# Kernel tuning notes

Hardware: AMD Instinct MI355X
Metric: run time of the kernel (lower is better)

Reference implementation:

```python
import jax, jax.numpy as jnp
import numpy as np

B, S, HID, NH, CACHE = 2, 1024, 1024, 16, 4096
HD = HID // NH
HOT = max(4, CACHE // 4)
COLD = CACHE - HOT
COMP = HID // 2
EPS = 1e-5


def setup_inputs() -> dict:
    key = jax.random.key(0)
    ks = jax.random.split(key, 16)
    std = 0.02
    inp = {
        'inputs': jax.random.normal(ks[0], (B, S, HID), jnp.float32),
        'hot_keys': std * jax.random.normal(ks[1], (HOT, HID), jnp.float32),
        'hot_values': std * jax.random.normal(ks[2], (HOT, HID), jnp.float32),
        'hot_age': jnp.zeros((HOT,), jnp.float32),
        'hot_access': jnp.zeros((HOT,), jnp.float32),
        'cold_keys': std * jax.random.normal(ks[3], (COLD, HID), jnp.float32),
        'cold_values': std * jax.random.normal(ks[4], (COLD, HID), jnp.float32),
        'cold_age': jnp.zeros((COLD,), jnp.float32),
        'cold_access': jnp.zeros((COLD,), jnp.float32),
        # linear weights stored [in, out] (y = x @ W + b)
        'Wq': std * jax.random.normal(ks[5], (HID, HID), jnp.float32),
        'bq': jnp.zeros((HID,), jnp.float32),
        'Wk': std * jax.random.normal(ks[6], (HID, HID), jnp.float32),
        'bk': jnp.zeros((HID,), jnp.float32),
        'Wv': std * jax.random.normal(ks[7], (HID, HID), jnp.float32),
        'bv': jnp.zeros((HID,), jnp.float32),
        'Wo': std * jax.random.normal(ks[8], (HID, HID), jnp.float32),
        'bo': jnp.zeros((HID,), jnp.float32),
        'Wc': (1.0 / np.sqrt(HID)) * jax.random.normal(ks[9], (HID, COMP), jnp.float32),
        'bc': jnp.zeros((COMP,), jnp.float32),
        'Wd': (1.0 / np.sqrt(COMP)) * jax.random.normal(ks[10], (COMP, HID), jnp.float32),
        'bd': jnp.zeros((HID,), jnp.float32),
        'gamma': jnp.ones((HID,), jnp.float32),
        'beta': jnp.zeros((HID,), jnp.float32),
    }
    return inp


def _cache_level(q, cache_k, v_flat, age, access, Wk, bk, Wo, bo):
    # q: [B, NH, S, HD]; cache_k/v_flat: [C, HID]
    C = cache_k.shape[0]
    k = (cache_k @ Wk + bk).reshape(C, NH, HD)
    v = v_flat.reshape(C, NH, HD)
    scores = jnp.einsum('bhsd,chd->bhsc', q, k) / np.sqrt(HD)
    scores = scores + (-0.1 * age + 0.05 * access)  # broadcast over [B,H,S,C]
    attn = jax.nn.softmax(scores, axis=-1)
    out = jnp.einsum('bhsc,chd->bhsd', attn, v)
    out = out.transpose(0, 2, 1, 3).reshape(q.shape[0], q.shape[2], HID)
    return out @ Wo + bo


def reference(inputs, hot_keys, hot_values, hot_age, hot_access,
              cold_keys, cold_values, cold_age, cold_access,
              Wq, bq, Wk, bk, Wv, bv, Wo, bo, Wc, bc, Wd, bd, gamma, beta):
    q = (inputs @ Wq + bq).reshape(B, S, NH, HD).transpose(0, 2, 1, 3)
    # hot tier: values through value_net
    hot_v = hot_values @ Wv + bv
    hot_out = _cache_level(q, hot_keys, hot_v, hot_age, hot_access, Wk, bk, Wo, bo)
    # cold tier: values through compressor -> decompressor
    cold_v = (cold_values @ Wc + bc) @ Wd + bd
    cold_out = _cache_level(q, cold_keys, cold_v, cold_age, cold_access, Wk, bk, Wo, bo)
    x = hot_out + cold_out
    mu = jnp.mean(x, axis=-1, keepdims=True)
    var = jnp.mean(jnp.square(x - mu), axis=-1, keepdims=True)
    return (x - mu) / jnp.sqrt(var + EPS) * gamma + beta
```

## Files before the change

### kernel.cpp

```cpp
#include <hip/hip_runtime.h>

#define BBATCH 2
#define SS   1024
#define HID  1024
#define NH   16
#define HD   64
#define HOT  1024
#define COLD 3072
#define COMP 512

typedef __attribute__((ext_vector_type(8))) short s8v;
typedef __attribute__((ext_vector_type(4))) float f4v;
typedef unsigned short u16;
typedef unsigned int   u32;

__device__ __forceinline__ float b2f(u16 u){ return __uint_as_float(((u32)u)<<16); }
__device__ __forceinline__ u16 f2b(float f){
  u32 u = __float_as_uint(f);
  u += 0x7FFF + ((u>>16)&1);
  return (u16)(u>>16);
}
__device__ __forceinline__ u32 pk2r(u32 a, u32 b){
  return __builtin_amdgcn_perm(b + 0x8000u, a + 0x8000u, 0x07060302u);
}
__device__ __forceinline__ float ldsc(const void* p, int i, int isf32){
  return isf32 ? ((const float*)p)[i] : b2f(((const u16*)p)[i]);
}

__global__ void detect_kernel(const u32* __restrict__ gamma_raw, u32* __restrict__ flag){
  if (threadIdx.x == 0) flag[0] = (gamma_raw[0] == 0x3F800000u) ? 1u : 0u;
}

__global__ __launch_bounds__(256) void bias_kernel(
    const void* __restrict__ h_age, const void* __restrict__ h_acc,
    const void* __restrict__ c_age, const void* __restrict__ c_acc,
    float* __restrict__ BiasH, float* __restrict__ BiasC, const u32* __restrict__ flag)
{
  const int f = (int)flag[0];
  const int i = blockIdx.x * 256 + threadIdx.x;
  if (i < HOT) BiasH[i] = -0.1f * ldsc(h_age, i, f) + 0.05f * ldsc(h_acc, i, f);
  const int j = i - HOT;
  if (j >= 0 && j < COLD) BiasC[j] = -0.1f * ldsc(c_age, j, f) + 0.05f * ldsc(c_acc, j, f);
}

struct CDesc { const void* S; u16* D; int tile0, pad; };
struct CBatch { CDesc d[5]; int nd; };

__global__ __launch_bounds__(256) void convert_multi(CBatch cb, const u32* __restrict__ flag)
{
  int di = 0;
  for (int i = 1; i < cb.nd; i++) if ((int)blockIdx.x >= cb.d[i].tile0) di = i;
  const CDesc g = cb.d[di];
  const int f = (int)flag[0];
  const size_t e0 = (size_t)(blockIdx.x - g.tile0) * 2048 + (size_t)threadIdx.x * 8;
  if (f) {
    const float* s = (const float*)g.S + e0;
    const uint4 x = *(const uint4*)s, y = *(const uint4*)(s + 4);
    *(uint4*)(g.D + e0) =
      (uint4){ pk2r(x.x,x.y), pk2r(x.z,x.w), pk2r(y.x,y.y), pk2r(y.z,y.w) };
  } else {
    *(uint4*)(g.D + e0) = *(const uint4*)((const u16*)g.S + e0);
  }
}

struct TDesc { const void* S; u16* D; int R, C, cshift, tile0; };
struct TBatch { TDesc d[6]; int nd; };

__global__ __launch_bounds__(256) void transpose_kernel(TBatch tb, const u32* __restrict__ flag)
{
  __shared__ __align__(16) u16 Tt[64][72];
  int di = 0;
  for (int i = 1; i < tb.nd; i++) if ((int)blockIdx.x >= tb.d[i].tile0) di = i;
  const TDesc g = tb.d[di];
  const int local = blockIdx.x - g.tile0;
  const int ty = local >> g.cshift;
  const int tx = local & ((1 << g.cshift) - 1);
  const int r0 = ty * 64, c0 = tx * 64;
  const int f = (int)flag[0];
  const int t = threadIdx.x;
  const int sr = t >> 2, sc = (t & 3) * 16;

  union { uint4 q[2]; u16 h[16]; } u;
  if (f) {
    const float* s = (const float*)g.S + (size_t)(r0 + sr) * g.C + c0 + sc;
    const uint4 a = *(const uint4*)s,     b = *(const uint4*)(s + 4);
    const uint4 c = *(const uint4*)(s + 8), d2 = *(const uint4*)(s + 12);
    u.q[0] = (uint4){ pk2r(a.x,a.y), pk2r(a.z,a.w), pk2r(b.x,b.y), pk2r(b.z,b.w) };
    u.q[1] = (uint4){ pk2r(c.x,c.y), pk2r(c.z,c.w), pk2r(d2.x,d2.y), pk2r(d2.z,d2.w) };
  } else {
    const u16* s = (const u16*)g.S + (size_t)(r0 + sr) * g.C + c0 + sc;
    u.q[0] = *(const uint4*)s;  u.q[1] = *(const uint4*)(s + 8);
  }
  #pragma unroll
  for (int i = 0; i < 16; i++) Tt[sc + i][sr] = u.h[i];
  __syncthreads();

  const int dc = t >> 2, dr = (t & 3) * 16;
  const uint4 o0 = *(const uint4*)&Tt[dc][dr];
  const uint4 o1 = *(const uint4*)&Tt[dc][dr + 8];
  u16* dp = g.D + (size_t)(c0 + dc) * g.R + r0 + dr;
  *(uint4*)dp = o0;  *(uint4*)(dp + 8) = o1;
}

#define BM 128
#define BN 64
#define BK 32
struct GemmDesc {
  const void* A; const u16* BT; const void* bias; u16* C;
  int aflag, bcol0, M, N, K, nxlog, tile0, ctrans;
  float bias_scale;
};
struct GemmBatch { GemmDesc d[6]; int nd; };

__global__ __launch_bounds__(256) void gemm_multi(GemmBatch bat, const u32* __restrict__ flag)
{
  __shared__ __align__(16) u16 As[BM][BK + 8];
  __shared__ __align__(16) u16 Bs[BN][BK + 8];

  int di = 0;
  for (int i = 1; i < bat.nd; i++) if ((int)blockIdx.x >= bat.d[i].tile0) di = i;
  const GemmDesc g = bat.d[di];
  const int local = blockIdx.x - g.tile0;
  const int ty = local >> g.nxlog;
  const int tx = local - (ty << g.nxlog);
  const int m0 = ty * BM, n0 = tx * BN;

  const int f  = (int)flag[0];
  const int af = g.aflag ? f : 0;

  const int tid  = threadIdx.x;
  const int lane = tid & 63, wave = tid >> 6;
  const int quad = lane >> 4, l15 = lane & 15;
  const int wy = wave >> 1, wx = wave & 1;

  f4v acc[4][2];
  #pragma unroll
  for (int i = 0; i < 4; i++)
    #pragma unroll
    for (int j = 0; j < 2; j++) acc[i][j] = (f4v){0.f,0.f,0.f,0.f};

  const int ar = tid >> 1, ac = (tid & 1) * 16;
  const int br = tid >> 2, bc = (tid & 3) * 8;

  uint4 a0, a1, a2, a3;
  uint4 b0;

  auto load_tile = [&](int kk) {
    if (af) {
      const float* s = (const float*)g.A + (size_t)(m0 + ar) * g.K + kk + ac;
      a0 = *(const uint4*)s;       a1 = *(const uint4*)(s + 4);
      a2 = *(const uint4*)(s + 8); a3 = *(const uint4*)(s + 12);
    } else {
      const u16* s = (const u16*)g.A + (size_t)(m0 + ar) * g.K + kk + ac;
      a0 = *(const uint4*)s;  a1 = *(const uint4*)(s + 8);
    }
    const u16* bs = g.BT + (size_t)(g.bcol0 + n0 + br) * g.K + kk + bc;
    b0 = *(const uint4*)bs;
  };

  load_tile(0);

  for (int k0 = 0; k0 < g.K; k0 += BK) {
    __syncthreads();
    if (af) {
      *(uint4*)&As[ar][ac] =
        (uint4){ pk2r(a0.x,a0.y), pk2r(a0.z,a0.w), pk2r(a1.x,a1.y), pk2r(a1.z,a1.w) };
      *(uint4*)&As[ar][ac + 8] =
        (uint4){ pk2r(a2.x,a2.y), pk2r(a2.z,a2.w), pk2r(a3.x,a3.y), pk2r(a3.z,a3.w) };
    } else {
      *(uint4*)&As[ar][ac] = a0;  *(uint4*)&As[ar][ac + 8] = a1;
    }
    *(uint4*)&Bs[br][bc] = b0;
    __syncthreads();

    if (k0 + BK < g.K) load_tile(k0 + BK);

    s8v afr[4], bfr[2];
    #pragma unroll
    for (int i = 0; i < 4; i++)
      afr[i] = *(const s8v*)&As[wy * 64 + i * 16 + l15][quad * 8];
    #pragma unroll
    for (int j = 0; j < 2; j++)
      bfr[j] = *(const s8v*)&Bs[wx * 32 + j * 16 + l15][quad * 8];

    #pragma unroll
    for (int j = 0; j < 2; j++)
      #pragma unroll
      for (int i = 0; i < 4; i++)
        acc[i][j] = __builtin_amdgcn_mfma_f32_16x16x32_bf16(afr[i], bfr[j], acc[i][j], 0, 0, 0);
  }

  if (g.ctrans) {
    #pragma unroll
    for (int j = 0; j < 2; j++) {
      const int col = n0 + wx * 32 + j * 16 + l15;
      const float bv = ldsc(g.bias, g.bcol0 + col, f) * g.bias_scale;
      #pragma unroll
      for (int i = 0; i < 4; i++) {
        const int row = m0 + wy * 64 + i * 16 + quad * 4;
        u16 t4[4];
        #pragma unroll
        for (int r = 0; r < 4; r++) t4[r] = f2b(acc[i][j][r] + bv);
        *(uint2*)&g.C[(size_t)col * g.M + row] = *(uint2*)t4;
      }
    }
  } else {
    #pragma unroll
    for (int j = 0; j < 2; j++) {
      const int col = n0 + wx * 32 + j * 16 + l15;
      const float bv = ldsc(g.bias, g.bcol0 + col, f) * g.bias_scale;
      #pragma unroll
      for (int i = 0; i < 4; i++) {
        const int row = m0 + wy * 64 + i * 16 + quad * 4;
        #pragma unroll
        for (int r = 0; r < 4; r++)
          g.C[(size_t)(row + r) * g.N + col] = f2b(acc[i][j][r] + bv);
      }
    }
  }
}

#define KV(row, blk) (((row) << 6) + ((((blk) ^ ((row) & 7))) << 3))

__global__ __launch_bounds__(256) void attn_kernel(
    const u16* __restrict__ Q,
    const u16* __restrict__ KHg, const u16* __restrict__ VHT,
    const u16* __restrict__ KCg, const u16* __restrict__ VCT,
    const float* __restrict__ BiasH, const float* __restrict__ BiasC,
    float* __restrict__ HotOut, float* __restrict__ ColdNum3, float* __restrict__ ColdZ3,
    int NG, int glog)
{
  __shared__ __align__(16) u16 Ks[64 * 64];
  __shared__ __align__(16) u16 Vs[64 * 64];

  const int tid  = threadIdx.x;
  const int lane = tid & 63, wave = tid >> 6;
  const int quad = lane >> 4, l15 = lane & 15;

  const int bx    = blockIdx.x;
  const int slice = bx & 3;
  const int sblk  = (bx >> 2) & 7;
  const int h     = (bx >> 5) & ((1 << glog) - 1);
  const int b     = bx >> (5 + glog);

  const int rowbase = b * SS + sblk * 128;
  const int hoff  = h * HD;
  const int myrow = wave * 32;

  const bool hot = (slice == 0);
  const u16*  Kt   = hot ? KHg : KCg;
  const u16*  Vt   = hot ? VHT : VCT;
  const float* Bias = hot ? BiasH : BiasC;
  const int   e0  = hot ? 0 : (slice - 1) * 1024;
  const int   ldv = hot ? HOT : COLD;

  const u16* qp = Q + (size_t)(rowbase + myrow + l15) * NG + hoff + quad * 8;
  const s8v aq0 = *(const s8v*)qp;
  const s8v aq1 = *(const s8v*)(qp + 32);
  const u16* qp1 = qp + (size_t)16 * NG;
  const s8v aq2 = *(const s8v*)qp1;
  const s8v aq3 = *(const s8v*)(qp1 + 32);

  const int rk = tid >> 2, cb2 = (tid & 3) * 2, sk = (tid & 3) * 16;
  const u16* kbase = Kt + (size_t)(e0 + rk) * NG + hoff + sk;
  const u16* vbase = Vt + (size_t)(hoff + rk) * ldv + e0 + sk;
  uint4 kr0 = *(const uint4*)kbase, kr1 = *(const uint4*)(kbase + 8);
  uint4 vr0 = *(const uint4*)vbase, vr1 = *(const uint4*)(vbase + 8);

  u16* kw0 = &Ks[KV(rk, cb2)];     u16* kw1 = &Ks[KV(rk, cb2 + 1)];
  u16* vw0 = &Vs[KV(rk, cb2)];     u16* vw1 = &Vs[KV(rk, cb2 + 1)];

  f4v o0[4], o1[4];
  #pragma unroll
  for (int j = 0; j < 4; j++) { o0[j] = (f4v){0.f,0.f,0.f,0.f}; o1[j] = (f4v){0.f,0.f,0.f,0.f}; }
  float zs0 = 0.f, zs1 = 0.f;

  for (int c0 = 0; c0 < 1024; c0 += 64) {
    __syncthreads();
    *(uint4*)kw0 = kr0;  *(uint4*)kw1 = kr1;
    *(uint4*)vw0 = vr0;  *(uint4*)vw1 = vr1;
    __syncthreads();
    if (c0 + 64 < 1024) {
      const u16* kn = kbase + (size_t)(c0 + 64) * NG;
      const u16* vn = vbase + (c0 + 64);
      kr0 = *(const uint4*)kn;  kr1 = *(const uint4*)(kn + 8);
      vr0 = *(const uint4*)vn;  vr1 = *(const uint4*)(vn + 8);
    }

    #pragma unroll
    for (int h2 = 0; h2 < 2; h2++) {
      const s8v ka0 = *(const s8v*)&Ks[KV(h2 * 32 + l15, quad)];
      const s8v ka1 = *(const s8v*)&Ks[KV(h2 * 32 + l15, 4 + quad)];
      const s8v kb0 = *(const s8v*)&Ks[KV(h2 * 32 + 16 + l15, quad)];
      const s8v kb1 = *(const s8v*)&Ks[KV(h2 * 32 + 16 + l15, 4 + quad)];

      const int cg0 = e0 + c0 + h2 * 32 + quad * 4;
      const float4 bi0 = *(const float4*)&Bias[cg0];
      const float4 bi1 = *(const float4*)&Bias[cg0 + 16];

      union { u32 w[4]; s8v v; } ap0, ap1;
      {
        f4v s0 = (f4v){0.f,0.f,0.f,0.f}, s1 = (f4v){0.f,0.f,0.f,0.f};
        s0 = __builtin_amdgcn_mfma_f32_16x16x32_bf16(ka0, aq0, s0, 0, 0, 0);
        s0 = __builtin_amdgcn_mfma_f32_16x16x32_bf16(ka1, aq1, s0, 0, 0, 0);
        s1 = __builtin_amdgcn_mfma_f32_16x16x32_bf16(kb0, aq0, s1, 0, 0, 0);
        s1 = __builtin_amdgcn_mfma_f32_16x16x32_bf16(kb1, aq1, s1, 0, 0, 0);
        float p0[4], p1[4];
        p0[0] = __expf(fminf(s0[0] * 0.125f + bi0.x, 30.f));
        p0[1] = __expf(fminf(s0[1] * 0.125f + bi0.y, 30.f));
        p0[2] = __expf(fminf(s0[2] * 0.125f + bi0.z, 30.f));
        p0[3] = __expf(fminf(s0[3] * 0.125f + bi0.w, 30.f));
        p1[0] = __expf(fminf(s1[0] * 0.125f + bi1.x, 30.f));
        p1[1] = __expf(fminf(s1[1] * 0.125f + bi1.y, 30.f));
        p1[2] = __expf(fminf(s1[2] * 0.125f + bi1.z, 30.f));
        p1[3] = __expf(fminf(s1[3] * 0.125f + bi1.w, 30.f));
        zs0 += p0[0] + p0[1] + p0[2] + p0[3] + p1[0] + p1[1] + p1[2] + p1[3];
        const u32 W0 = pk2r(__float_as_uint(p0[0]), __float_as_uint(p0[1]));
        const u32 W1 = pk2r(__float_as_uint(p0[2]), __float_as_uint(p0[3]));
        const u32 W2 = pk2r(__float_as_uint(p1[0]), __float_as_uint(p1[1]));
        const u32 W3 = pk2r(__float_as_uint(p1[2]), __float_as_uint(p1[3]));
        #pragma unroll
        for (int t = 0; t < 4; t++) {
          const int srcl = (((quad << 1) + (t >> 1)) & 3) * 16 + l15;
          const u32 lo = __shfl((t & 1) ? W1 : W0, srcl, 64);
          const u32 hi = __shfl((t & 1) ? W3 : W2, srcl, 64);
          ap0.w[t] = (quad >= 2) ? hi : lo;
        }
      }
      {
        f4v s0 = (f4v){0.f,0.f,0.f,0.f}, s1 = (f4v){0.f,0.f,0.f,0.f};
        s0 = __builtin_amdgcn_mfma_f32_16x16x32_bf16(ka0, aq2, s0, 0, 0, 0);
        s0 = __builtin_amdgcn_mfma_f32_16x16x32_bf16(ka1, aq3, s0, 0, 0, 0);
        s1 = __builtin_amdgcn_mfma_f32_16x16x32_bf16(kb0, aq2, s1, 0, 0, 0);
        s1 = __builtin_amdgcn_mfma_f32_16x16x32_bf16(kb1, aq3, s1, 0, 0, 0);
        float p0[4], p1[4];
        p0[0] = __expf(fminf(s0[0] * 0.125f + bi0.x, 30.f));
        p0[1] = __expf(fminf(s0[1] * 0.125f + bi0.y, 30.f));
        p0[2] = __expf(fminf(s0[2] * 0.125f + bi0.z, 30.f));
        p0[3] = __expf(fminf(s0[3] * 0.125f + bi0.w, 30.f));
        p1[0] = __expf(fminf(s1[0] * 0.125f + bi1.x, 30.f));
        p1[1] = __expf(fminf(s1[1] * 0.125f + bi1.y, 30.f));
        p1[2] = __expf(fminf(s1[2] * 0.125f + bi1.z, 30.f));
        p1[3] = __expf(fminf(s1[3] * 0.125f + bi1.w, 30.f));
        zs1 += p0[0] + p0[1] + p0[2] + p0[3] + p1[0] + p1[1] + p1[2] + p1[3];
        const u32 W0 = pk2r(__float_as_uint(p0[0]), __float_as_uint(p0[1]));
        const u32 W1 = pk2r(__float_as_uint(p0[2]), __float_as_uint(p0[3]));
        const u32 W2 = pk2r(__float_as_uint(p1[0]), __float_as_uint(p1[1]));
        const u32 W3 = pk2r(__float_as_uint(p1[2]), __float_as_uint(p1[3]));
        #pragma unroll
        for (int t = 0; t < 4; t++) {
          const int srcl = (((quad << 1) + (t >> 1)) & 3) * 16 + l15;
          const u32 lo = __shfl((t & 1) ? W1 : W0, srcl, 64);
          const u32 hi = __shfl((t & 1) ? W3 : W2, srcl, 64);
          ap1.w[t] = (quad >= 2) ? hi : lo;
        }
      }
      #pragma unroll
      for (int j2 = 0; j2 < 4; j2++) {
        const s8v bv = *(const s8v*)&Vs[KV(j2 * 16 + l15, h2 * 4 + quad)];
        o0[j2] = __builtin_amdgcn_mfma_f32_16x16x32_bf16(ap0.v, bv, o0[j2], 0, 0, 0);
        o1[j2] = __builtin_amdgcn_mfma_f32_16x16x32_bf16(ap1.v, bv, o1[j2], 0, 0, 0);
      }
    }
  }

  zs0 += __shfl_xor(zs0, 16, 64);  zs0 += __shfl_xor(zs0, 32, 64);
  zs1 += __shfl_xor(zs1, 16, 64);  zs1 += __shfl_xor(zs1, 32, 64);

  if (hot) {
    float rz0[4], rz1[4];
    #pragma unroll
    for (int r = 0; r < 4; r++) {
      rz0[r] = 1.0f / __shfl(zs0, quad * 4 + r, 64);
      rz1[r] = 1.0f / __shfl(zs1, quad * 4 + r, 64);
    }
    #pragma unroll
    for (int j = 0; j < 4; j++) {
      const int col = hoff + j * 16 + l15;
      #pragma unroll
      for (int r = 0; r < 4; r++) {
        const int row = rowbase + myrow + quad * 4 + r;
        HotOut[(size_t)row * NG + col]        = o0[j][r] * rz0[r];
        HotOut[(size_t)(row + 16) * NG + col] = o1[j][r] * rz1[r];
      }
    }
  } else {
    float* CN = ColdNum3 + (size_t)(slice - 1) * 2048 * NG;
    #pragma unroll
    for (int j = 0; j < 4; j++) {
      const int col = hoff + j * 16 + l15;
      #pragma unroll
      for (int r = 0; r < 4; r++) {
        const int row = rowbase + myrow + quad * 4 + r;
        CN[(size_t)row * NG + col]        = o0[j][r];
        CN[(size_t)(row + 16) * NG + col] = o1[j][r];
      }
    }
    if (lane < 16) {
      const size_t zb = (size_t)(slice - 1) * 2048 + rowbase + myrow;
      ColdZ3[(zb + lane) * (1 << glog) + h]      = zs0;
      ColdZ3[(zb + 16 + lane) * (1 << glog) + h] = zs1;
    }
  }
}

__global__ __launch_bounds__(256) void combine_kernel(
    const float* __restrict__ HotOut, const float* __restrict__ ColdNum3,
    const float* __restrict__ ColdZ3, u16* __restrict__ ATT,
    int att_ld, int att_c0, int NG, int glog)
{
  const int gid   = blockIdx.x * 256 + threadIdx.x;
  const int shift = 4 + glog;
  const int row   = gid >> shift;
  const int c4    = (gid & ((1 << shift) - 1)) << 2;
  const int h     = c4 >> 6;
  const int G     = 1 << glog;
  const size_t ps = (size_t)2048 * NG;
  const size_t zs = (size_t)2048 * G;

  const float4 hv = *(const float4*)&HotOut[(size_t)row * NG + c4];
  const float4 c1 = *(const float4*)&ColdNum3[(size_t)row * NG + c4];
  const float4 c2 = *(const float4*)&ColdNum3[ps + (size_t)row * NG + c4];
  const float4 c3 = *(const float4*)&ColdNum3[2 * ps + (size_t)row * NG + c4];
  const float z = ColdZ3[(size_t)row * G + h] + ColdZ3[zs + (size_t)row * G + h]
                + ColdZ3[2 * zs + (size_t)row * G + h];
  const float zi = 1.0f / z;

  u16 ov[4];
  ov[0] = f2b(hv.x + (c1.x + c2.x + c3.x) * zi);
  ov[1] = f2b(hv.y + (c1.y + c2.y + c3.y) * zi);
  ov[2] = f2b(hv.z + (c1.z + c2.z + c3.z) * zi);
  ov[3] = f2b(hv.w + (c1.w + c2.w + c3.w) * zi);
  *(uint2*)&ATT[(size_t)row * att_ld + att_c0 + c4] = *(uint2*)ov;
}

__global__ __launch_bounds__(256) void ln_kernel(
    const u16* __restrict__ X, const void* __restrict__ gamma,
    const void* __restrict__ beta, void* __restrict__ outp,
    const u32* __restrict__ flag)
{
  __shared__ float red[4];
  const int f = (int)flag[0];
  const int row = blockIdx.x, tid = threadIdx.x;
  const u16* xr = X + (size_t)row * HID;

  float x[4];
  { union { uint2 q; u16 hx[4]; } bx2;
    bx2.q = *(const uint2*)(xr + tid * 4);
    #pragma unroll
    for (int i = 0; i < 4; i++) x[i] = b2f(bx2.hx[i]); }

  float s = x[0] + x[1] + x[2] + x[3];
  #pragma unroll
  for (int m = 1; m < 64; m <<= 1) s += __shfl_xor(s, m, 64);
  if ((tid & 63) == 0) red[tid >> 6] = s;
  __syncthreads();
  const float mu = (red[0] + red[1] + red[2] + red[3]) * (1.0f / HID);
  __syncthreads();

  float v = 0.f;
  #pragma unroll
  for (int i = 0; i < 4; i++) { const float d = x[i] - mu; v += d * d; }
  #pragma unroll
  for (int m = 1; m < 64; m <<= 1) v += __shfl_xor(v, m, 64);
  if ((tid & 63) == 0) red[tid >> 6] = v;
  __syncthreads();
  const float var  = (red[0] + red[1] + red[2] + red[3]) * (1.0f / HID);
  const float rstd = 1.0f / sqrtf(var + 1e-5f);

  #pragma unroll
  for (int i = 0; i < 4; i++) {
    const int col = tid * 4 + i;
    const float val = (x[i] - mu) * rstd * ldsc(gamma, col, f) + ldsc(beta, col, f);
    if (f) ((float*)outp)[(size_t)row * HID + col] = val;
    else   ((u16*) outp)[(size_t)row * HID + col] = f2b(val);
  }
}

extern "C" void kernel_launch(void* const* d_in, const int* in_sizes, int n_in,
                              void* d_out, int out_size, void* d_ws, size_t ws_size,
                              hipStream_t stream)
{
  const void* inputs      = d_in[0];
  const void* hot_keys    = d_in[1];
  const void* hot_values  = d_in[2];
  const void* hot_age     = d_in[3];
  const void* hot_access  = d_in[4];
  const void* cold_keys   = d_in[5];
  const void* cold_values = d_in[6];
  const void* cold_age    = d_in[7];
  const void* cold_access = d_in[8];
  const void* Wq = d_in[9];   const void* bq = d_in[10];
  const void* Wk = d_in[11];  const void* bk = d_in[12];
  const void* Wv = d_in[13];  const void* bv = d_in[14];
  const void* Wo = d_in[15];  const void* bo = d_in[16];
  const void* Wc = d_in[17];  const void* bc = d_in[18];
  const void* Wd = d_in[19];  const void* bd = d_in[20];
  const void* gamma = d_in[21];
  const void* beta  = d_in[22];

  const size_t FIX    = 256 + 16384;
  const size_t WT     = (size_t)10 * 1024 * 1024;
  const size_t COPIES = (size_t)10240 * 1024 * 2;
  const size_t XB     = (size_t)2048 * HID * 2;
  auto PART = [](int Gc){ return (size_t)2048 * (64 * Gc) * 16 + (size_t)2048 * Gc * 12; };
  auto BUFS = [](int Gc){ return (size_t)10240 * (64 * Gc) * 2; };
  auto MX   = [](size_t a, size_t b){ return a > b ? a : b; };

  int G = 0, docopy = 0;
  { const size_t needF = FIX + WT + MX(COPIES, MX(PART(16), XB)) + BUFS(16);
    if (ws_size >= needF) { G = 16; docopy = 1; } }
  for (int c = 8; c >= 2 && !G; c >>= 1)
    if (ws_size >= FIX + WT + COPIES + MX(PART(c), XB) + BUFS(c)) { G = c; docopy = 1; }
  for (int c = 8; c >= 2 && !G; c >>= 1)
    if (ws_size >= FIX + WT + MX(PART(c), XB) + BUFS(c)) { G = c; docopy = 0; }
  if (!G) return;
  const int glog = (G == 16) ? 4 : (G == 8 ? 3 : (G == 4 ? 2 : 1));
  const int NG = 64 * G;
  const bool full = (G == 16);

  char* base  = (char*)d_ws;
  u32*  flag  = (u32*)base;
  float* BiasH = (float*)(base + 256);
  float* BiasC = BiasH + HOT;
  u16* WqT = (u16*)(base + FIX);
  u16* WkT = WqT + (size_t)1024 * 1024;
  u16* WvT = WkT + (size_t)1024 * 1024;
  u16* WoT = WvT + (size_t)1024 * 1024;
  u16* WcT = WoT + (size_t)1024 * 1024;
  u16* WdT = WcT + (size_t)512 * 1024;
  char* rp0 = base + FIX + WT;

  u16* inputsB = (u16*)rp0;
  u16* hotkB   = inputsB + (size_t)2048 * 1024;
  u16* coldkB  = hotkB   + (size_t)1024 * 1024;
  u16* hotvB   = coldkB  + (size_t)3072 * 1024;
  u16* coldvB  = hotvB   + (size_t)1024 * 1024;

  char* rp = rp0 + ((docopy && !full) ? COPIES : 0);
  u16*   X        = (u16*)rp;
  float* HotOut   = (float*)rp;
  float* ColdNum3 = (float*)(rp + (size_t)2048 * NG * 4);
  float* ColdZ3   = (float*)(rp + (size_t)2048 * NG * 16);
  const size_t Rbytes = full ? MX(COPIES, MX(PART(16), XB)) : MX(PART(G), XB);
  u16* Qg  = (u16*)(rp + Rbytes);
  u16* KHg = Qg  + (size_t)2048 * NG;
  u16* KCg = KHg + (size_t)HOT  * NG;
  u16* VHT = KCg + (size_t)COLD * NG;
  u16* VCT = VHT + (size_t)HOT  * NG;
  u16* ATT   = (u16*)d_out;
  u16* CVmid = (u16*)d_out + (size_t)2048 * 1024;

  const void* Aq = docopy ? (const void*)inputsB : inputs;
  const void* Ahk = docopy ? (const void*)hotkB  : hot_keys;
  const void* Ack = docopy ? (const void*)coldkB : cold_keys;
  const void* Ahv = docopy ? (const void*)hotvB  : hot_values;
  const void* Acv = docopy ? (const void*)coldvB : cold_values;
  const int afl = docopy ? 0 : 1;

  const dim3 blk(256);
  const int mQ = 2048 / BM, mH = HOT / BM, mC = COLD / BM;

  detect_kernel<<<dim3(1), dim3(64), 0, stream>>>((const u32*)gamma, flag);
  bias_kernel<<<dim3((HOT + COLD) / 256), blk, 0, stream>>>(
      hot_age, hot_access, cold_age, cold_access, BiasH, BiasC, flag);

  if (docopy) {
    CBatch cb; cb.nd = 5; int t = 0;
    cb.d[0] = { inputs,      inputsB, t, 0 }; t += 1024;
    cb.d[1] = { hot_keys,    hotkB,   t, 0 }; t += 512;
    cb.d[2] = { cold_keys,   coldkB,  t, 0 }; t += 1536;
    cb.d[3] = { hot_values,  hotvB,   t, 0 }; t += 512;
    cb.d[4] = { cold_values, coldvB,  t, 0 }; t += 1536;
    convert_multi<<<dim3(t), blk, 0, stream>>>(cb, flag);
  }
  { TBatch tb; tb.nd = 6; int t = 0;
    tb.d[0] = { Wq, WqT, 1024, 1024, 4, t }; t += 256;
    tb.d[1] = { Wk, WkT, 1024, 1024, 4, t }; t += 256;
    tb.d[2] = { Wv, WvT, 1024, 1024, 4, t }; t += 256;
    tb.d[3] = { Wo, WoT, 1024, 1024, 4, t }; t += 256;
    tb.d[4] = { Wc, WcT, 1024,  512, 3, t }; t += 128;
    tb.d[5] = { Wd, WdT,  512, 1024, 4, t }; t += 128;
    transpose_kernel<<<dim3(t), blk, 0, stream>>>(tb, flag);
  }

  if (full) {
    { GemmBatch bb; bb.nd = 5; int t = 0;
      bb.d[0] = { Aq,  WqT, bq, Qg,    afl, 0, 2048, 1024, 1024, 4, t, 0, 1.0f }; t += 16 * mQ;
      bb.d[1] = { Ahk, WkT, bk, KHg,   afl, 0, HOT,  1024, 1024, 4, t, 0, 1.0f }; t += 16 * mH;
      bb.d[2] = { Ack, WkT, bk, KCg,   afl, 0, COLD, 1024, 1024, 4, t, 0, 1.0f }; t += 16 * mC;
      bb.d[3] = { Ahv, WvT, bv, VHT,   afl, 0, HOT,  1024, 1024, 4, t, 1, 1.0f }; t += 16 * mH;
      bb.d[4] = { Acv, WcT, bc, CVmid, afl, 0, COLD,  512, 1024, 3, t, 0, 1.0f }; t += 8 * mC;
      gemm_multi<<<dim3(t), blk, 0, stream>>>(bb, flag);
    }
    { GemmBatch bb; bb.nd = 1;
      bb.d[0] = { CVmid, WdT, bd, VCT, 0, 0, COLD, 1024, 512, 4, 0, 1, 1.0f };
      gemm_multi<<<dim3(16 * mC), blk, 0, stream>>>(bb, flag);
    }
    attn_kernel<<<dim3(BBATCH * 16 * 8 * 4), blk, 0, stream>>>(
        Qg, KHg, VHT, KCg, VCT, BiasH, BiasC, HotOut, ColdNum3, ColdZ3, NG, glog);
    combine_kernel<<<dim3((2048 * (NG / 4)) / 256), blk, 0, stream>>>(
        HotOut, ColdNum3, ColdZ3, ATT, HID, 0, NG, glog);
  } else {
    { GemmBatch bb; bb.nd = 5; int t = 0;
      bb.d[0] = { Aq,  WqT, bq, Qg,    afl, 0, 2048, NG,  1024, glog, t, 0, 1.0f }; t += G * mQ;
      bb.d[1] = { Ahk, WkT, bk, KHg,   afl, 0, HOT,  NG,  1024, glog, t, 0, 1.0f }; t += G * mH;
      bb.d[2] = { Ack, WkT, bk, KCg,   afl, 0, COLD, NG,  1024, glog, t, 0, 1.0f }; t += G * mC;
      bb.d[3] = { Ahv, WvT, bv, VHT,   afl, 0, HOT,  NG,  1024, glog, t, 1, 1.0f }; t += G * mH;
      bb.d[4] = { Acv, WcT, bc, CVmid, afl, 0, COLD, 512, 1024, 3,    t, 0, 1.0f }; t += 8 * mC;
      gemm_multi<<<dim3(t), blk, 0, stream>>>(bb, flag);
    }
    { GemmBatch bb; bb.nd = 1;
      bb.d[0] = { CVmid, WdT, bd, VCT, 0, 0, COLD, NG, 512, glog, 0, 1, 1.0f };
      gemm_multi<<<dim3(G * mC), blk, 0, stream>>>(bb, flag);
    }
    attn_kernel<<<dim3(BBATCH * G * 8 * 4), blk, 0, stream>>>(
        Qg, KHg, VHT, KCg, VCT, BiasH, BiasC, HotOut, ColdNum3, ColdZ3, NG, glog);
    combine_kernel<<<dim3((2048 * (NG / 4)) / 256), blk, 0, stream>>>(
        HotOut, ColdNum3, ColdZ3, ATT, HID, 0, NG, glog);

    for (int p = 1; p < NH / G; ++p) {
      const int c0 = p * NG;
      GemmBatch bb; bb.nd = 5; int t = 0;
      bb.d[0] = { Aq,    WqT, bq, Qg,  afl, c0, 2048, NG, 1024, glog, t, 0, 1.0f }; t += G * mQ;
      bb.d[1] = { Ahk,   WkT, bk, KHg, afl, c0, HOT,  NG, 1024, glog, t, 0, 1.0f }; t += G * mH;
      bb.d[2] = { Ack,   WkT, bk, KCg, afl, c0, COLD, NG, 1024, glog, t, 0, 1.0f }; t += G * mC;
      bb.d[3] = { Ahv,   WvT, bv, VHT, afl, c0, HOT,  NG, 1024, glog, t, 1, 1.0f }; t += G * mH;
      bb.d[4] = { CVmid, WdT, bd, VCT, 0,   c0, COLD, NG, 512,  glog, t, 1, 1.0f }; t += G * mC;
      gemm_multi<<<dim3(t), blk, 0, stream>>>(bb, flag);

      attn_kernel<<<dim3(BBATCH * G * 8 * 4), blk, 0, stream>>>(
          Qg, KHg, VHT, KCg, VCT, BiasH, BiasC, HotOut, ColdNum3, ColdZ3, NG, glog);
      combine_kernel<<<dim3((2048 * (NG / 4)) / 256), blk, 0, stream>>>(
          HotOut, ColdNum3, ColdZ3, ATT, HID, c0, NG, glog);
    }
  }

  { GemmBatch bb; bb.nd = 1;
    bb.d[0] = { ATT, WoT, bo, X, 0, 0, 2048, 1024, 1024, 4, 0, 0, 2.0f };
    gemm_multi<<<dim3(16 * mQ), blk, 0, stream>>>(bb, flag);
  }
  ln_kernel<<<dim3(2048), blk, 0, stream>>>(X, gamma, beta, d_out, flag);
}
```

Measured before the change: 311.1 us.

## Load GEMM bf16 tiles directly into LDS with swizzled unpadded layout

Replaces the register-staged global-to-LDS copies of bf16 A and B tiles with global_load_lds direct transfers, and changes the shared tiles from padded rows to an XOR-swizzled layout to avoid bank conflicts. The fp32 A path keeps register staging but writes into the swizzled layout. Removing the register prefetch means the bf16 path no longer overlaps the next tile's global load with MFMA compute, since loads are issued right before the barrier. This may expose load latency.

```diff
diff --git a/kernel.cpp b/kernel.cpp
--- a/kernel.cpp
+++ b/kernel.cpp
@@ -25,6 +25,11 @@
 }
 __device__ __forceinline__ float ldsc(const void* p, int i, int isf32){
   return isf32 ? ((const float*)p)[i] : b2f(((const u16*)p)[i]);
+}
+__device__ __forceinline__ void gl16(const u16* g, u16* l){
+  __builtin_amdgcn_global_load_lds(
+      (const __attribute__((address_space(1))) u32*)g,
+      (__attribute__((address_space(3))) u32*)l, 16, 0, 0);
 }
 
 __global__ void detect_kernel(const u32* __restrict__ gamma_raw, u32* __restrict__ flag){
@@ -105,6 +110,8 @@
 #define BM 128
 #define BN 64
 #define BK 32
+#define GSW(row, blk) (((row) << 5) + ((((blk) ^ (((row) >> 1) & 3))) << 3))
+
 struct GemmDesc {
   const void* A; const u16* BT; const void* bias; u16* C;
   int aflag, bcol0, M, N, K, nxlog, tile0, ctrans;
@@ -114,8 +121,8 @@
 
 __global__ __launch_bounds__(256) void gemm_multi(GemmBatch bat, const u32* __restrict__ flag)
 {
-  __shared__ __align__(16) u16 As[BM][BK + 8];
-  __shared__ __align__(16) u16 Bs[BN][BK + 8];
+  __shared__ __align__(16) u16 As[BM * BK];
+  __shared__ __align__(16) u16 Bs[BN * BK];
 
   int di = 0;
   for (int i = 1; i < bat.nd; i++) if ((int)blockIdx.x >= bat.d[i].tile0) di = i;
@@ -139,49 +146,53 @@
     #pragma unroll
     for (int j = 0; j < 2; j++) acc[i][j] = (f4v){0.f,0.f,0.f,0.f};
 
+  const int lrow = lane >> 2, lpos = lane & 3;
+  const int arow0 = wave * 32 + lrow, arow1 = arow0 + 16;
+  const int brow  = wave * 16 + lrow;
+  const u16* gA0 = (const u16*)g.A + (size_t)(m0 + arow0) * g.K + ((lpos ^ ((arow0 >> 1) & 3)) << 3);
+  const u16* gA1 = (const u16*)g.A + (size_t)(m0 + arow1) * g.K + ((lpos ^ ((arow1 >> 1) & 3)) << 3);
+  const u16* gB0 = g.BT + (size_t)(g.bcol0 + n0 + brow) * g.K + ((lpos ^ ((brow >> 1) & 3)) << 3);
+  u16* lA0 = &As[wave * 1024];
+  u16* lA1 = &As[wave * 1024 + 512];
+  u16* lB0 = &Bs[wave * 512];
+
   const int ar = tid >> 1, ac = (tid & 1) * 16;
-  const int br = tid >> 2, bc = (tid & 3) * 8;
-
+  const int sAr = (ar >> 1) & 3, b0i = (tid & 1) * 2;
   uint4 a0, a1, a2, a3;
-  uint4 b0;
-
-  auto load_tile = [&](int kk) {
-    if (af) {
-      const float* s = (const float*)g.A + (size_t)(m0 + ar) * g.K + kk + ac;
-      a0 = *(const uint4*)s;       a1 = *(const uint4*)(s + 4);
-      a2 = *(const uint4*)(s + 8); a3 = *(const uint4*)(s + 12);
-    } else {
-      const u16* s = (const u16*)g.A + (size_t)(m0 + ar) * g.K + kk + ac;
-      a0 = *(const uint4*)s;  a1 = *(const uint4*)(s + 8);
-    }
-    const u16* bs = g.BT + (size_t)(g.bcol0 + n0 + br) * g.K + kk + bc;
-    b0 = *(const uint4*)bs;
+  auto load_Aregs = [&](int kk) {
+    const float* s = (const float*)g.A + (size_t)(m0 + ar) * g.K + kk + ac;
+    a0 = *(const uint4*)s;       a1 = *(const uint4*)(s + 4);
+    a2 = *(const uint4*)(s + 8); a3 = *(const uint4*)(s + 12);
   };
-
-  load_tile(0);
+  if (af) load_Aregs(0);
 
   for (int k0 = 0; k0 < g.K; k0 += BK) {
     __syncthreads();
     if (af) {
-      *(uint4*)&As[ar][ac] =
+      *(uint4*)&As[(ar << 5) + (((b0i    ) ^ sAr) << 3)] =
         (uint4){ pk2r(a0.x,a0.y), pk2r(a0.z,a0.w), pk2r(a1.x,a1.y), pk2r(a1.z,a1.w) };
-      *(uint4*)&As[ar][ac + 8] =
+      *(uint4*)&As[(ar << 5) + (((b0i + 1) ^ sAr) << 3)] =
         (uint4){ pk2r(a2.x,a2.y), pk2r(a2.z,a2.w), pk2r(a3.x,a3.y), pk2r(a3.z,a3.w) };
     } else {
-      *(uint4*)&As[ar][ac] = a0;  *(uint4*)&As[ar][ac + 8] = a1;
-    }
-    *(uint4*)&Bs[br][bc] = b0;
+      gl16(gA0 + k0, lA0);
+      gl16(gA1 + k0, lA1);
+    }
+    gl16(gB0 + k0, lB0);
     __syncthreads();
 
-    if (k0 + BK < g.K) load_tile(k0 + BK);
+    if (af && k0 + BK < g.K) load_Aregs(k0 + BK);
 
     s8v afr[4], bfr[2];
     #pragma unroll
-    for (int i = 0; i < 4; i++)
-      afr[i] = *(const s8v*)&As[wy * 64 + i * 16 + l15][quad * 8];
-    #pragma unroll
-    for (int j = 0; j < 2; j++)
-      bfr[j] = *(const s8v*)&Bs[wx * 32 + j * 16 + l15][quad * 8];
+    for (int i = 0; i < 4; i++) {
+      const int rr = wy * 64 + i * 16 + l15;
+      afr[i] = *(const s8v*)&As[GSW(rr, quad)];
+    }
+    #pragma unroll
+    for (int j = 0; j < 2; j++) {
+      const int rb = wx * 32 + j * 16 + l15;
+      bfr[j] = *(const s8v*)&Bs[GSW(rb, quad)];
+    }
 
     #pragma unroll
     for (int j = 0; j < 2; j++)
```

Result: faster. 302.1 us (-2.9%).
